# Optimization experiments

Hardware: AMD Instinct MI355X
Metric: run time of the kernel (lower is better)

Reference implementation:

```python
import jax, jax.numpy as jnp
import numpy as np

ELT_BATCH = 64            # number of candidate elements (rows)
OBS_PER_ELT = 100_000     # observations per element (uniform row_lengths)
DATA_SIZE = ELT_BATCH * OBS_PER_ELT
THRESH_DEG = 2.0
THRESH_HIT_PROB_POST = 0.95


def _deg2dist(deg):
    # chord length on unit sphere subtended by angle `deg`
    return 2.0 * np.sin(np.radians(deg) / 2.0)


def setup_inputs() -> dict:
    key = jax.random.key(0)
    k1, k2, k3, k4 = jax.random.split(key, 4)
    # observed unit directions
    u_obs = jax.random.normal(k1, (DATA_SIZE, 3), dtype=jnp.float32)
    u_obs = u_obs / jnp.linalg.norm(u_obs, axis=-1, keepdims=True)
    # predicted directions = observed + small perturbation so a realistic
    # fraction of observations fall inside the 2-degree threshold
    noise = 0.01 * jax.random.normal(k2, (DATA_SIZE, 3), dtype=jnp.float32)
    u_pred = u_obs + noise
    u_pred = u_pred / jnp.linalg.norm(u_pred, axis=-1, keepdims=True)
    # mixture-model params per element: hit fraction h in (0.1, 0.9), decay lam in (1, 10)
    h = 0.1 + 0.8 * jax.random.uniform(k3, (ELT_BATCH,), dtype=jnp.float32)
    lam = 1.0 + 9.0 * jax.random.uniform(k4, (ELT_BATCH,), dtype=jnp.float32)
    # squared chord-distance threshold per element (constant buffer in the layer)
    thresh_s2 = jnp.full((ELT_BATCH,), np.float32(_deg2dist(THRESH_DEG) ** 2), dtype=jnp.float32)
    return {"u_pred": u_pred, "u_obs": u_obs, "h": h, "lam": lam, "thresh_s2": thresh_s2}


def reference(u_pred, u_obs, h, lam, thresh_s2):
    B = thresh_s2.shape[0]
    n_per = u_pred.shape[0] // B  # uniform row_lengths
    seg_ids = jnp.repeat(jnp.arange(B, dtype=jnp.int32), n_per)  # [data_size]

    # squared chord distance per observation
    du = u_pred - u_obs                                # [N, 3]
    s2 = jnp.sum(jnp.square(du), axis=-1)              # [N]

    thresh_rep = jnp.repeat(thresh_s2, n_per)          # [N]
    h_rep = jnp.repeat(h, n_per)                       # [N]
    lam_rep = jnp.repeat(lam, n_per)                   # [N]

    is_close = s2 < thresh_rep                         # [N] bool
    v = s2 / thresh_rep                                # normalized squared distance in [0,1) where close

    # truncated-exponential mixture model
    emlx = jnp.exp(-lam_rep * v)
    p_hit_cond = emlx * lam_rep / (1.0 - jnp.exp(-lam_rep))
    p_hit = h_rep * p_hit_cond
    p = p_hit + (1.0 - h_rep)

    # mask instead of boolean_mask: excluded entries contribute 0 to segment sums
    log_p = jnp.where(is_close, jnp.log(p), 0.0)
    p_hit_post = p_hit / p
    is_real_hit = p_hit_post > THRESH_HIT_PROB_POST
    p_hit_filtered = jnp.where(is_close & is_real_hit, p_hit_post, 0.0)

    log_like = jax.ops.segment_sum(log_p, seg_ids, num_segments=B)        # [B]
    hits = jax.ops.segment_sum(p_hit_filtered, seg_ids, num_segments=B)   # [B]
    hits_raw = hits  # original code sums p_hit_filtered for both outputs
    return (log_like, hits, hits_raw)
```

## Files before the change

### kernel.cpp

```cpp
#include <hip/hip_runtime.h>


constexpr int ELT_BATCH     = 64;
constexpr int OBS_PER_ELT   = 100000;
constexpr int GROUPS_PER_SEG = OBS_PER_ELT / 4;
constexpr int F4_PER_SEG     = OBS_PER_ELT * 3 / 4;
constexpr int BLOCKS_PER_SEG = 32;
constexpr int BLOCK          = 256;

__device__ __forceinline__ float wave_reduce_sum(float v) {
    #pragma unroll
    for (int off = 32; off > 0; off >>= 1)
        v += __shfl_down(v, off, 64);
    return v;
}

__global__ __launch_bounds__(BLOCK) void TrajectoryScore_58145267253396_kernel(
    const float4* __restrict__ pred4,
    const float4* __restrict__ obs4,
    const float*  __restrict__ h_arr,
    const float*  __restrict__ lam_arr,
    const float*  __restrict__ th_arr,
    float*        __restrict__ out)
{
    const int seg        = blockIdx.x / BLOCKS_PER_SEG;
    const int blk_in_seg = blockIdx.x % BLOCKS_PER_SEG;
    const int tid        = threadIdx.x;

    const float h      = h_arr[seg];
    const float lam    = lam_arr[seg];
    const float th     = th_arr[seg];
    const float inv_th = 1.0f / th;
    const float coef   = h * lam / (1.0f - __expf(-lam));
    const float omh    = 1.0f - h;
    const float nli    = -lam * inv_th;

    float ll = 0.0f;
    float hs = 0.0f;

    const int seg_base = seg * F4_PER_SEG;

    for (int g = blk_in_seg * BLOCK + tid; g < GROUPS_PER_SEG; g += BLOCKS_PER_SEG * BLOCK) {
        const int base = seg_base + g * 3;
        const float4 a0 = pred4[base], a1 = pred4[base + 1], a2 = pred4[base + 2];
        const float4 b0 = obs4[base],  b1 = obs4[base + 1],  b2 = obs4[base + 2];

        float dx, dy, dz, s2[4];
        dx = a0.x - b0.x; dy = a0.y - b0.y; dz = a0.z - b0.z;
        s2[0] = dx * dx + dy * dy + dz * dz;
        dx = a0.w - b0.w; dy = a1.x - b1.x; dz = a1.y - b1.y;
        s2[1] = dx * dx + dy * dy + dz * dz;
        dx = a1.z - b1.z; dy = a1.w - b1.w; dz = a2.x - b2.x;
        s2[2] = dx * dx + dy * dy + dz * dz;
        dx = a2.y - b2.y; dy = a2.z - b2.z; dz = a2.w - b2.w;
        s2[3] = dx * dx + dy * dy + dz * dz;

        #pragma unroll
        for (int k = 0; k < 4; ++k) {
            const float s     = s2[k];
            const float e     = __expf(nli * s);
            const float p_hit = coef * e;
            const float p     = p_hit + omh;
            const bool  close = s < th;
            const float lp    = __logf(p);
            ll += close ? lp : 0.0f;
            const float post  = p_hit / p;
            hs += (close && post > 0.95f) ? post : 0.0f;
        }
    }

    ll = wave_reduce_sum(ll);
    hs = wave_reduce_sum(hs);

    __shared__ float sll[BLOCK / 64];
    __shared__ float shs[BLOCK / 64];
    const int wave = tid >> 6;
    const int lane = tid & 63;
    if (lane == 0) { sll[wave] = ll; shs[wave] = hs; }
    __syncthreads();
    if (tid == 0) {
        float L = 0.0f, H = 0.0f;
        #pragma unroll
        for (int w = 0; w < BLOCK / 64; ++w) { L += sll[w]; H += shs[w]; }
        atomicAdd(&out[seg], L);
        atomicAdd(&out[ELT_BATCH + seg], H);
        atomicAdd(&out[2 * ELT_BATCH + seg], H);
    }
}

extern "C" void kernel_launch(void* const* d_in, const int* in_sizes, int n_in,
                              void* d_out, int out_size, void* d_ws, size_t ws_size,
                              hipStream_t stream) {
    const float4* pred4  = (const float4*)d_in[0];
    const float4* obs4   = (const float4*)d_in[1];
    const float*  h_arr  = (const float*)d_in[2];
    const float*  lam_arr = (const float*)d_in[3];
    const float*  th_arr = (const float*)d_in[4];
    float* out = (float*)d_out;

    hipMemsetAsync(out, 0, out_size * sizeof(float), stream);

    dim3 grid(ELT_BATCH * BLOCKS_PER_SEG);
    dim3 block(BLOCK);
    TrajectoryScore_58145267253396_kernel<<<grid, block, 0, stream>>>(
        pred4, obs4, h_arr, lam_arr, th_arr, out);
}
```

Measured before the change: 178.4 us.

## Fully unroll per-thread work with batched 12-byte loads for more loads in flight

Replaces the strided float4 grouped loop with a fixed, fully unrolled schedule: each thread handles 12 observations at stride of the per-segment thread count, issuing six pred/obs load pairs per batch before computing, plus a tail. Loads switch from float4 triples to 12-byte struct loads, each coalesced across the wavefront. The intent is to raise memory-level parallelism and remove loop overhead, at the cost of more registers and non-16-byte-aligned loads.

Result: no change. 178.5 us (+0.1%).

```diff
diff --git a/kernel.cpp b/kernel.cpp
--- a/kernel.cpp
+++ b/kernel.cpp
@@ -1,12 +1,34 @@
 #include <hip/hip_runtime.h>
 
 
-constexpr int ELT_BATCH     = 64;
-constexpr int OBS_PER_ELT   = 100000;
-constexpr int GROUPS_PER_SEG = OBS_PER_ELT / 4;
-constexpr int F4_PER_SEG     = OBS_PER_ELT * 3 / 4;
+constexpr int ELT_BATCH      = 64;
+constexpr int OBS_PER_ELT    = 100000;
+constexpr int BLOCK          = 256;
 constexpr int BLOCKS_PER_SEG = 32;
-constexpr int BLOCK          = 256;
+constexpr int TPS            = BLOCK * BLOCKS_PER_SEG;
+constexpr int FULL_ITERS     = OBS_PER_ELT / TPS;
+constexpr int TAIL           = OBS_PER_ELT - FULL_ITERS * TPS;
+
+struct F3 { float x, y, z; };
+
+__device__ __forceinline__ void process_obs(
+    const F3 a, const F3 b,
+    const float th, const float nli, const float coef, const float omh,
+    float& ll, float& hs)
+{
+    const float dx = a.x - b.x;
+    const float dy = a.y - b.y;
+    const float dz = a.z - b.z;
+    const float s2 = dx * dx + dy * dy + dz * dz;
+    const float e     = __expf(nli * s2);
+    const float p_hit = coef * e;
+    const float p     = p_hit + omh;
+    const bool  close = s2 < th;
+    const float lp    = __logf(p);
+    ll += close ? lp : 0.0f;
+    const float post  = p_hit / p;
+    hs += (close && post > 0.95f) ? post : 0.0f;
+}
 
 __device__ __forceinline__ float wave_reduce_sum(float v) {
     #pragma unroll
@@ -16,57 +38,45 @@
 }
 
 __global__ __launch_bounds__(BLOCK) void TrajectoryScore_58145267253396_kernel(
-    const float4* __restrict__ pred4,
-    const float4* __restrict__ obs4,
-    const float*  __restrict__ h_arr,
-    const float*  __restrict__ lam_arr,
-    const float*  __restrict__ th_arr,
-    float*        __restrict__ out)
+    const F3*    __restrict__ pred,
+    const F3*    __restrict__ obs,
+    const float* __restrict__ h_arr,
+    const float* __restrict__ lam_arr,
+    const float* __restrict__ th_arr,
+    float*       __restrict__ out)
 {
-    const int seg        = blockIdx.x / BLOCKS_PER_SEG;
-    const int blk_in_seg = blockIdx.x % BLOCKS_PER_SEG;
-    const int tid        = threadIdx.x;
+    const int seg = blockIdx.x / BLOCKS_PER_SEG;
+    const int g   = (blockIdx.x % BLOCKS_PER_SEG) * BLOCK + threadIdx.x;
 
-    const float h      = h_arr[seg];
-    const float lam    = lam_arr[seg];
-    const float th     = th_arr[seg];
-    const float inv_th = 1.0f / th;
-    const float coef   = h * lam / (1.0f - __expf(-lam));
-    const float omh    = 1.0f - h;
-    const float nli    = -lam * inv_th;
+    const float h    = h_arr[seg];
+    const float lam  = lam_arr[seg];
+    const float th   = th_arr[seg];
+    const float coef = h * lam / (1.0f - __expf(-lam));
+    const float omh  = 1.0f - h;
+    const float nli  = -lam / th;
 
     float ll = 0.0f;
     float hs = 0.0f;
 
-    const int seg_base = seg * F4_PER_SEG;
+    const int base = seg * OBS_PER_ELT + g;
 
-    for (int g = blk_in_seg * BLOCK + tid; g < GROUPS_PER_SEG; g += BLOCKS_PER_SEG * BLOCK) {
-        const int base = seg_base + g * 3;
-        const float4 a0 = pred4[base], a1 = pred4[base + 1], a2 = pred4[base + 2];
-        const float4 b0 = obs4[base],  b1 = obs4[base + 1],  b2 = obs4[base + 2];
+    #pragma unroll
+    for (int half = 0; half < 2; ++half) {
+        F3 a[6], b[6];
+        #pragma unroll
+        for (int j = 0; j < 6; ++j) {
+            const int idx = base + (half * 6 + j) * TPS;
+            a[j] = pred[idx];
+            b[j] = obs[idx];
+        }
+        #pragma unroll
+        for (int j = 0; j < 6; ++j)
+            process_obs(a[j], b[j], th, nli, coef, omh, ll, hs);
+    }
 
-        float dx, dy, dz, s2[4];
-        dx = a0.x - b0.x; dy = a0.y - b0.y; dz = a0.z - b0.z;
-        s2[0] = dx * dx + dy * dy + dz * dz;
-        dx = a0.w - b0.w; dy = a1.x - b1.x; dz = a1.y - b1.y;
-        s2[1] = dx * dx + dy * dy + dz * dz;
-        dx = a1.z - b1.z; dy = a1.w - b1.w; dz = a2.x - b2.x;
-        s2[2] = dx * dx + dy * dy + dz * dz;
-        dx = a2.y - b2.y; dy = a2.z - b2.z; dz = a2.w - b2.w;
-        s2[3] = dx * dx + dy * dy + dz * dz;
-
-        #pragma unroll
-        for (int k = 0; k < 4; ++k) {
-            const float s     = s2[k];
-            const float e     = __expf(nli * s);
-            const float p_hit = coef * e;
-            const float p     = p_hit + omh;
-            const bool  close = s < th;
-            const float lp    = __logf(p);
-            ll += close ? lp : 0.0f;
-            const float post  = p_hit / p;
-            hs += (close && post > 0.95f) ? post : 0.0f;
-        }
+    if (g < TAIL) {
+        const int idx = base + FULL_ITERS * TPS;
+        process_obs(pred[idx], obs[idx], th, nli, coef, omh, ll, hs);
     }
 
     ll = wave_reduce_sum(ll);
@@ -74,11 +84,11 @@
 
     __shared__ float sll[BLOCK / 64];
     __shared__ float shs[BLOCK / 64];
-    const int wave = tid >> 6;
-    const int lane = tid & 63;
+    const int wave = threadIdx.x >> 6;
+    const int lane = threadIdx.x & 63;
     if (lane == 0) { sll[wave] = ll; shs[wave] = hs; }
     __syncthreads();
-    if (tid == 0) {
+    if (threadIdx.x == 0) {
         float L = 0.0f, H = 0.0f;
         #pragma unroll
         for (int w = 0; w < BLOCK / 64; ++w) { L += sll[w]; H += shs[w]; }
@@ -91,11 +101,11 @@
 extern "C" void kernel_launch(void* const* d_in, const int* in_sizes, int n_in,
                               void* d_out, int out_size, void* d_ws, size_t ws_size,
                               hipStream_t stream) {
-    const float4* pred4  = (const float4*)d_in[0];
-    const float4* obs4   = (const float4*)d_in[1];
-    const float*  h_arr  = (const float*)d_in[2];
-    const float*  lam_arr = (const float*)d_in[3];
-    const float*  th_arr = (const float*)d_in[4];
+    const F3*    pred    = (const F3*)d_in[0];
+    const F3*    obs     = (const F3*)d_in[1];
+    const float* h_arr   = (const float*)d_in[2];
+    const float* lam_arr = (const float*)d_in[3];
+    const float* th_arr  = (const float*)d_in[4];
     float* out = (float*)d_out;
 
     hipMemsetAsync(out, 0, out_size * sizeof(float), stream);
@@ -103,5 +113,5 @@
     dim3 grid(ELT_BATCH * BLOCKS_PER_SEG);
     dim3 block(BLOCK);
     TrajectoryScore_58145267253396_kernel<<<grid, block, 0, stream>>>(
-        pred4, obs4, h_arr, lam_arr, th_arr, out);
+        pred, obs, h_arr, lam_arr, th_arr, out);
 }
```

## Stage squared differences through shared memory with coalesced per-block tiles

Applied to the files above, without the earlier changes.

Each block now owns a contiguous tile of 1000 observations (750 float4 per input), which every thread loads with fully coalesced float4 reads. Each thread squares the component differences and writes them to shared memory, so that later threads can regroup them per observation. Before, each thread read three strided float4 per group in a grid-stride loop, so each wave's accesses were spread out. The grid grows from 32 to 100 blocks per segment with one pass per block. The cost is a shared-memory staging step, a block barrier, and stride-3 LDS reads that may cause bank conflicts.

After: 185.9 us. 1.04x slower.

```diff
diff --git a/kernel.cpp b/kernel.cpp
--- a/kernel.cpp
+++ b/kernel.cpp
@@ -1,12 +1,13 @@
 #include <hip/hip_runtime.h>
 
 
-constexpr int ELT_BATCH     = 64;
-constexpr int OBS_PER_ELT   = 100000;
-constexpr int GROUPS_PER_SEG = OBS_PER_ELT / 4;
+constexpr int ELT_BATCH      = 64;
+constexpr int OBS_PER_ELT    = 100000;
 constexpr int F4_PER_SEG     = OBS_PER_ELT * 3 / 4;
-constexpr int BLOCKS_PER_SEG = 32;
 constexpr int BLOCK          = 256;
+constexpr int BLOCKS_PER_SEG = 100;
+constexpr int F4_PER_BLOCK   = F4_PER_SEG / BLOCKS_PER_SEG;
+constexpr int OBS_PER_BLOCK  = OBS_PER_ELT / BLOCKS_PER_SEG;
 
 __device__ __forceinline__ float wave_reduce_sum(float v) {
     #pragma unroll
@@ -23,45 +24,55 @@
     const float*  __restrict__ th_arr,
     float*        __restrict__ out)
 {
-    const int seg        = blockIdx.x / BLOCKS_PER_SEG;
-    const int blk_in_seg = blockIdx.x % BLOCKS_PER_SEG;
-    const int tid        = threadIdx.x;
+    __shared__ float q2[F4_PER_BLOCK * 4];
 
-    const float h      = h_arr[seg];
-    const float lam    = lam_arr[seg];
-    const float th     = th_arr[seg];
-    const float inv_th = 1.0f / th;
-    const float coef   = h * lam / (1.0f - __expf(-lam));
-    const float omh    = 1.0f - h;
-    const float nli    = -lam * inv_th;
+    const int seg     = blockIdx.x / BLOCKS_PER_SEG;
+    const int blk     = blockIdx.x % BLOCKS_PER_SEG;
+    const int tid     = threadIdx.x;
+    const int f4_base = seg * F4_PER_SEG + blk * F4_PER_BLOCK;
+
+    float4 a[3], b[3];
+    #pragma unroll
+    for (int k = 0; k < 3; ++k) {
+        const int idx = tid + k * BLOCK;
+        if (idx < F4_PER_BLOCK) {
+            a[k] = pred4[f4_base + idx];
+            b[k] = obs4[f4_base + idx];
+        }
+    }
+
+    const float h    = h_arr[seg];
+    const float lam  = lam_arr[seg];
+    const float th   = th_arr[seg];
+    const float coef = h * lam / (1.0f - __expf(-lam));
+    const float omh  = 1.0f - h;
+    const float nli  = -lam / th;
+
+    #pragma unroll
+    for (int k = 0; k < 3; ++k) {
+        const int idx = tid + k * BLOCK;
+        if (idx < F4_PER_BLOCK) {
+            float4 d;
+            d.x = a[k].x - b[k].x; d.y = a[k].y - b[k].y;
+            d.z = a[k].z - b[k].z; d.w = a[k].w - b[k].w;
+            float4 s;
+            s.x = d.x * d.x; s.y = d.y * d.y; s.z = d.z * d.z; s.w = d.w * d.w;
+            reinterpret_cast<float4*>(q2)[idx] = s;
+        }
+    }
+    __syncthreads();
 
     float ll = 0.0f;
     float hs = 0.0f;
-
-    const int seg_base = seg * F4_PER_SEG;
-
-    for (int g = blk_in_seg * BLOCK + tid; g < GROUPS_PER_SEG; g += BLOCKS_PER_SEG * BLOCK) {
-        const int base = seg_base + g * 3;
-        const float4 a0 = pred4[base], a1 = pred4[base + 1], a2 = pred4[base + 2];
-        const float4 b0 = obs4[base],  b1 = obs4[base + 1],  b2 = obs4[base + 2];
-
-        float dx, dy, dz, s2[4];
-        dx = a0.x - b0.x; dy = a0.y - b0.y; dz = a0.z - b0.z;
-        s2[0] = dx * dx + dy * dy + dz * dz;
-        dx = a0.w - b0.w; dy = a1.x - b1.x; dz = a1.y - b1.y;
-        s2[1] = dx * dx + dy * dy + dz * dz;
-        dx = a1.z - b1.z; dy = a1.w - b1.w; dz = a2.x - b2.x;
-        s2[2] = dx * dx + dy * dy + dz * dz;
-        dx = a2.y - b2.y; dy = a2.z - b2.z; dz = a2.w - b2.w;
-        s2[3] = dx * dx + dy * dy + dz * dz;
-
-        #pragma unroll
-        for (int k = 0; k < 4; ++k) {
-            const float s     = s2[k];
-            const float e     = __expf(nli * s);
+    #pragma unroll
+    for (int k = 0; k < 4; ++k) {
+        const int t = tid + k * BLOCK;
+        if (t < OBS_PER_BLOCK) {
+            const float s2    = q2[3 * t] + q2[3 * t + 1] + q2[3 * t + 2];
+            const float e     = __expf(nli * s2);
             const float p_hit = coef * e;
             const float p     = p_hit + omh;
-            const bool  close = s < th;
+            const bool  close = s2 < th;
             const float lp    = __logf(p);
             ll += close ? lp : 0.0f;
             const float post  = p_hit / p;
@@ -91,11 +102,11 @@
 extern "C" void kernel_launch(void* const* d_in, const int* in_sizes, int n_in,
                               void* d_out, int out_size, void* d_ws, size_t ws_size,
                               hipStream_t stream) {
-    const float4* pred4  = (const float4*)d_in[0];
-    const float4* obs4   = (const float4*)d_in[1];
-    const float*  h_arr  = (const float*)d_in[2];
+    const float4* pred4   = (const float4*)d_in[0];
+    const float4* obs4    = (const float4*)d_in[1];
+    const float*  h_arr   = (const float*)d_in[2];
     const float*  lam_arr = (const float*)d_in[3];
-    const float*  th_arr = (const float*)d_in[4];
+    const float*  th_arr  = (const float*)d_in[4];
     float* out = (float*)d_out;
 
     hipMemsetAsync(out, 0, out_size * sizeof(float), stream);
```
